# Kernel tuning notes

Measured on AMD Instinct MI355X. Metric: run time of the kernel, lower is better.

Reference implementation:

```python
import jax, jax.numpy as jnp
import numpy as np

EMBED_DIM = 768
MAX_LEN = 1024
ALPHA = 0.99
BATCH = 16


def setup_inputs() -> dict:
    key = jax.random.key(0)
    k1, k2, k3 = jax.random.split(key, 3)
    x = jax.random.normal(k1, (BATCH, MAX_LEN, EMBED_DIM), dtype=jnp.float32)
    # torch nn.Linear(embed_dim, 3*embed_dim): store weight as [in, out] for x @ W
    scale = 1.0 / np.sqrt(EMBED_DIM)
    W_qkv = jax.random.uniform(k2, (EMBED_DIM, 3 * EMBED_DIM), dtype=jnp.float32,
                               minval=-scale, maxval=scale)
    b_qkv = jax.random.uniform(k3, (3 * EMBED_DIM,), dtype=jnp.float32,
                               minval=-scale, maxval=scale)
    return {"x": x, "W_qkv": W_qkv, "b_qkv": b_qkv}


def _retention_mask(sl, alpha, dtype):
    # M[i, j] = alpha**(i - j) if i >= j else 0 (causal tril * decay)
    i = jnp.arange(sl)[:, None]
    j = jnp.arange(sl)[None, :]
    causal = i >= j
    # compute decay only where causal to avoid huge alpha**(negative) values
    exponent = jnp.where(causal, (i - j).astype(dtype), 0.0)
    decay = jnp.asarray(alpha, dtype) ** exponent
    return jnp.where(causal, decay, jnp.zeros((), dtype))


def reference(x, W_qkv, b_qkv):
    bs, sl, d = x.shape
    qkv = x @ W_qkv + b_qkv                      # [B, S, 3D]
    q, k, v = jnp.split(qkv, 3, axis=-1)         # each [B, S, D]
    M = _retention_mask(sl, ALPHA, x.dtype)      # [S, S]
    scores = jnp.einsum('bsd,btd->bst', q, k) / jnp.sqrt(jnp.asarray(d, x.dtype))
    out = jnp.einsum('bst,btd->bsd', scores * M[None, :, :], v)
    return out
```

## Files before the change

### kernel.cpp

```cpp
#include <hip/hip_runtime.h>
#include <hip/hip_bf16.h>


#define SEQ   1024
#define DIM   768
#define ND3   2304

typedef __attribute__((ext_vector_type(8))) short bf16x8;
typedef __attribute__((ext_vector_type(4))) float f32x4;

#define L2A     (-0.014499569695115089f)
#define RSQRTD  (0.03608439182435161f)

__device__ __forceinline__ unsigned short f2bf(float x) {
  union { float f; unsigned u; } v; v.f = x;
  unsigned r = v.u + 0x7FFFu + ((v.u >> 16) & 1u);
  return (unsigned short)(r >> 16);
}

__device__ __forceinline__ void gload16(const void* g, void* l) {
  __builtin_amdgcn_global_load_lds(
      (const __attribute__((address_space(1))) void*)g,
      (__attribute__((address_space(3))) void*)l, 16, 0, 0);
}

__global__ void prep(const float* __restrict__ x, unsigned short* __restrict__ xb,
                     const float* __restrict__ W, unsigned short* __restrict__ Wt) {
  __shared__ float tile[64][65];
  int bid = blockIdx.x;
  if (bid < 6144) {
    size_t i = ((size_t)bid * 256 + threadIdx.x) * 8;
    float4 f0 = *(const float4*)(x + i);
    float4 f1 = *(const float4*)(x + i + 4);
    bf16x8 v;
    v[0] = (short)f2bf(f0.x); v[1] = (short)f2bf(f0.y);
    v[2] = (short)f2bf(f0.z); v[3] = (short)f2bf(f0.w);
    v[4] = (short)f2bf(f1.x); v[5] = (short)f2bf(f1.y);
    v[6] = (short)f2bf(f1.z); v[7] = (short)f2bf(f1.w);
    *(bf16x8*)(xb + i) = v;
  } else {
    int tb = bid - 6144;
    int n0 = (tb % 36) * 64;
    int k0 = (tb / 36) * 64;
    int tx = threadIdx.x & 63, ty = threadIdx.x >> 6;
#pragma unroll
    for (int p = 0; p < 16; ++p) {
      int k = ty + p * 4;
      tile[k][tx] = W[(size_t)(k0 + k) * ND3 + n0 + tx];
    }
    __syncthreads();
#pragma unroll
    for (int p = 0; p < 16; ++p) {
      int n = ty + p * 4;
      Wt[(size_t)(n0 + n) * DIM + k0 + tx] = f2bf(tile[tx][n]);
    }
  }
}

__global__ void __launch_bounds__(512, 4) qkv_g(
    const unsigned short* __restrict__ xb, const unsigned short* __restrict__ Wt,
    const float* __restrict__ bias,
    unsigned short* __restrict__ Qs, unsigned short* __restrict__ Ks,
    unsigned short* __restrict__ Vt) {
  __shared__ __align__(1024) char lsA[16384];
  __shared__ __align__(1024) char lsB[32768];
  int bid = (blockIdx.x & 7) * 144 + (blockIdx.x >> 3);
  int mt = bid / 9, ntb = bid % 9;
  int m0 = mt * 128, n0 = ntb * 256;

  int tid = threadIdx.x, lane = tid & 63, wid = tid >> 6;
  int lr = lane & 15, lg = lane >> 4;
  int wm = wid >> 2, wn = wid & 3;
  int c8 = (lane & 7) ^ (lane >> 3);
  int rloc = (lane >> 3) * 2 + (c8 >> 2), colo = (c8 & 3) * 8;
  const unsigned short* gA = xb + (size_t)(m0 + rloc) * DIM + colo;
  const unsigned short* gB = Wt + (size_t)(n0 + rloc) * DIM + colo;
  int slot16 = (((((lr & 1) << 2) | lg) ^ ((lr >> 1) & 7)) << 4);
  int rdA = wm * 4096 + (lr >> 1) * 128 + slot16;
  int rdB = wn * 4096 + (lr >> 1) * 128 + slot16;

  f32x4 acc[4][4] = {};

#define STG(t, par) do {                                                      \
    char* la_ = lsA + (par) * 8192;                                           \
    char* lb_ = lsB + (par) * 16384;                                          \
    gload16(gA + (size_t)(wid * 16) * DIM + (t) * 32, la_ + wid * 1024);      \
    gload16(gB + (size_t)(wid * 32) * DIM + (t) * 32, lb_ + wid * 2048);      \
    gload16(gB + (size_t)(wid * 32 + 16) * DIM + (t) * 32,                    \
            lb_ + wid * 2048 + 1024);                                         \
  } while (0)

  STG(0, 0);
  STG(1, 1);
  asm volatile("s_waitcnt vmcnt(3)" ::: "memory");
  __builtin_amdgcn_s_barrier();
  asm volatile("" ::: "memory");

  for (int t = 0; t < 24; ++t) {
    int pA = (t & 1) * 8192, pB = (t & 1) * 16384;
    bf16x8 aF[4], bF[4];
#pragma unroll
    for (int f = 0; f < 4; ++f)
      aF[f] = *(const bf16x8*)(lsA + pA + rdA + f * 1024);
#pragma unroll
    for (int n = 0; n < 4; ++n)
      bF[n] = *(const bf16x8*)(lsB + pB + rdB + n * 1024);
    __builtin_amdgcn_s_setprio(1);
#pragma unroll
    for (int f = 0; f < 4; ++f)
#pragma unroll
      for (int n = 0; n < 4; ++n)
        acc[f][n] = __builtin_amdgcn_mfma_f32_16x16x32_bf16(aF[f], bF[n], acc[f][n], 0, 0, 0);
    __builtin_amdgcn_s_setprio(0);

    if (t == 23) break;
    __builtin_amdgcn_s_barrier();
    asm volatile("" ::: "memory");
    if (t + 2 < 24) {
      STG(t + 2, t & 1);
      asm volatile("s_waitcnt vmcnt(3)" ::: "memory");
    } else {
      asm volatile("s_waitcnt vmcnt(0)" ::: "memory");
    }
    __builtin_amdgcn_s_barrier();
    asm volatile("" ::: "memory");
  }
#undef STG

  float bia[4];
#pragma unroll
  for (int n = 0; n < 4; ++n) bia[n] = bias[n0 + wn * 64 + n * 16 + lr];

  if (ntb < 3) {
#pragma unroll
    for (int f = 0; f < 4; ++f)
#pragma unroll
      for (int r = 0; r < 4; ++r) {
        int mg = m0 + wm * 64 + f * 16 + lg * 4 + r;
        int b = mg >> 10, s = mg & 1023;
        float sc = exp2f((float)s * L2A) * RSQRTD;
        unsigned short* dst = Qs + ((size_t)b * SEQ + s) * DIM + n0 + wn * 64 + lr;
#pragma unroll
        for (int n = 0; n < 4; ++n)
          dst[n * 16] = f2bf((acc[f][n][r] + bia[n]) * sc);
      }
  } else if (ntb < 6) {
#pragma unroll
    for (int f = 0; f < 4; ++f)
#pragma unroll
      for (int r = 0; r < 4; ++r) {
        int mg = m0 + wm * 64 + f * 16 + lg * 4 + r;
        int b = mg >> 10, s = mg & 1023;
        float sc = exp2f(-(float)s * L2A);
        unsigned short* dst = Ks + ((size_t)b * SEQ + s) * DIM + (n0 - DIM) + wn * 64 + lr;
#pragma unroll
        for (int n = 0; n < 4; ++n)
          dst[n * 16] = f2bf((acc[f][n][r] + bia[n]) * sc);
      }
  } else {
#pragma unroll
    for (int f = 0; f < 4; ++f) {
      int mg = m0 + wm * 64 + f * 16 + lg * 4;
      int b = mg >> 10, s0 = mg & 1023;
#pragma unroll
      for (int n = 0; n < 4; ++n) {
        int d = (n0 - 2 * DIM) + wn * 64 + n * 16 + lr;
        ushort4 v;
        v.x = f2bf(acc[f][n][0] + bia[n]);
        v.y = f2bf(acc[f][n][1] + bia[n]);
        v.z = f2bf(acc[f][n][2] + bia[n]);
        v.w = f2bf(acc[f][n][3] + bia[n]);
        *(ushort4*)(Vt + ((size_t)b * DIM + d) * SEQ + s0) = v;
      }
    }
  }
}

__device__ __forceinline__ void gemm_core(
    const unsigned short* gA, const unsigned short* gA2,
    const unsigned short* gB, const unsigned short* gB2,
    char* lsA, char* lsB, int nt, int wid, int lane, f32x4 acc[2][4]) {
  int lr = lane & 15, lg = lane >> 4;
  int wm = wid >> 1, wn = wid & 1;
  int rdA = (wm * 32 + lr) * 128 + ((lg ^ (lr & 7)) << 4);
  int rdB = (wn * 64 + lr) * 128 + ((lg ^ (lr & 7)) << 4);
  int wo = wid * 2048;

#define STAGE(t, par) do {                                                    \
    int lo_ = ((par) << 14) + wo;                                             \
    gload16(gA  + (size_t)(t) * 64, lsA + lo_);                               \
    gload16(gA2 + (size_t)(t) * 64, lsA + lo_ + 1024);                        \
    gload16(gB  + (size_t)(t) * 64, lsB + lo_);                               \
    gload16(gB2 + (size_t)(t) * 64, lsB + lo_ + 1024);                        \
  } while (0)

  STAGE(0, 0);
  STAGE(1, 1);
  asm volatile("s_waitcnt vmcnt(4)" ::: "memory");
  __builtin_amdgcn_s_barrier();
  asm volatile("" ::: "memory");

  for (int t = 0; t < nt; ++t) {
    int pbase = (t & 1) << 14;
    bf16x8 aF[2][2], bF[2][4];
#pragma unroll
    for (int kh = 0; kh < 2; ++kh) {
#pragma unroll
      for (int f = 0; f < 2; ++f)
        aF[kh][f] = *(const bf16x8*)(lsA + pbase + ((rdA + f * 2048) ^ (kh << 6)));
#pragma unroll
      for (int n = 0; n < 4; ++n)
        bF[kh][n] = *(const bf16x8*)(lsB + pbase + ((rdB + n * 2048) ^ (kh << 6)));
    }
    __builtin_amdgcn_s_setprio(1);
#pragma unroll
    for (int kh = 0; kh < 2; ++kh)
#pragma unroll
      for (int f = 0; f < 2; ++f)
#pragma unroll
        for (int n = 0; n < 4; ++n)
          acc[f][n] = __builtin_amdgcn_mfma_f32_16x16x32_bf16(aF[kh][f], bF[kh][n], acc[f][n], 0, 0, 0);
    __builtin_amdgcn_s_setprio(0);

    if (t == nt - 1) break;
    __builtin_amdgcn_s_barrier();
    asm volatile("" ::: "memory");
    if (t + 2 < nt) {
      STAGE(t + 2, t & 1);
      asm volatile("s_waitcnt vmcnt(4)" ::: "memory");
    } else {
      asm volatile("s_waitcnt vmcnt(0)" ::: "memory");
    }
    __builtin_amdgcn_s_barrier();
    asm volatile("" ::: "memory");
  }
#undef STAGE
}

__global__ void __launch_bounds__(512, 4) score_g(
    const unsigned short* __restrict__ Qs, const unsigned short* __restrict__ Ks,
    unsigned short* __restrict__ Sm, int b_base) {
  __shared__ __align__(1024) char lsA[32768];
  __shared__ __align__(1024) char lsB[32768];
  int bid = (blockIdx.x & 7) * (gridDim.x >> 3) + (blockIdx.x >> 3);
  int t = bid % 36, bl = bid / 36;
  int b = b_base + bl;
  int it = 0;
  while (t >= it + 1) { t -= it + 1; it++; }
  int jt = t;
  int m0 = it * 128, n0 = jt * 128;
  const unsigned short* A  = Qs + (size_t)b * SEQ * DIM;
  const unsigned short* Bt = Ks + (size_t)b * SEQ * DIM;
  unsigned short* Smp = Sm + (size_t)bl * SEQ * SEQ;

  int tid = threadIdx.x, lane = tid & 63, wid = tid >> 6;
  int l8 = lane >> 3, cs = ((lane & 7) ^ l8) << 3;
  int srow = wid * 16 + l8;

  const unsigned short* gA = A  + (size_t)(m0 + srow) * DIM + cs;
  const unsigned short* gB = Bt + (size_t)(n0 + srow) * DIM + cs;

  f32x4 acc[2][4] = {};
  gemm_core(gA, gA + 8 * DIM, gB, gB + 8 * DIM, lsA, lsB, 12, wid, lane, acc);

  int wm = wid >> 1, wn = wid & 1;
  int lr = lane & 15, lg = lane >> 4;
#pragma unroll
  for (int f = 0; f < 2; ++f)
#pragma unroll
    for (int n = 0; n < 4; ++n) {
      int j = n0 + wn * 64 + n * 16 + lr;
#pragma unroll
      for (int r = 0; r < 4; ++r) {
        int i = m0 + wm * 32 + f * 16 + lg * 4 + r;
        float v = acc[f][n][r];
        if (j > i) v = 0.0f;
        Smp[(size_t)i * SEQ + j] = f2bf(v);
      }
    }
}

__global__ void __launch_bounds__(512, 4) pv_g(
    const unsigned short* __restrict__ Sm, const unsigned short* __restrict__ Vt,
    float* __restrict__ out, int b_base, int gsz) {
  __shared__ __align__(1024) char lsA[32768];
  __shared__ __align__(1024) char lsB[32768];
  int it = 7 - blockIdx.x / (gsz * 6);
  int rem = blockIdx.x % (gsz * 6);
  int bl = rem / 6, dt = rem % 6;
  int b = b_base + bl;
  int m0 = it * 128, n0 = dt * 128;
  const unsigned short* A  = Sm + (size_t)bl * SEQ * SEQ;
  const unsigned short* Bt = Vt + (size_t)b * DIM * SEQ;
  int nt = (it + 1) * 2;

  int tid = threadIdx.x, lane = tid & 63, wid = tid >> 6;
  int l8 = lane >> 3, cs = ((lane & 7) ^ l8) << 3;
  int srow = wid * 16 + l8;

  const unsigned short* gA = A  + (size_t)(m0 + srow) * SEQ + cs;
  const unsigned short* gB = Bt + (size_t)(n0 + srow) * SEQ + cs;

  f32x4 acc[2][4] = {};
  gemm_core(gA, gA + 8 * SEQ, gB, gB + 8 * SEQ, lsA, lsB, nt, wid, lane, acc);

  int wm = wid >> 1, wn = wid & 1;
  int lr = lane & 15, lg = lane >> 4;
#pragma unroll
  for (int f = 0; f < 2; ++f)
#pragma unroll
    for (int n = 0; n < 4; ++n) {
      int d = n0 + wn * 64 + n * 16 + lr;
#pragma unroll
      for (int r = 0; r < 4; ++r) {
        int i = m0 + wm * 32 + f * 16 + lg * 4 + r;
        out[((size_t)b * SEQ + i) * DIM + d] = acc[f][n][r];
      }
    }
}

extern "C" void kernel_launch(void* const* d_in, const int* in_sizes, int n_in,
                              void* d_out, int out_size, void* d_ws, size_t ws_size,
                              hipStream_t stream) {
  const float* x    = (const float*)d_in[0];
  const float* W    = (const float*)d_in[1];
  const float* bias = (const float*)d_in[2];
  float* out = (float*)d_out;

  char* ws = (char*)d_ws;
  unsigned short* Wt = (unsigned short*)(ws);
  unsigned short* Qs = (unsigned short*)(ws + 3538944);
  unsigned short* Ks = (unsigned short*)(ws + 3538944 + 25165824);
  unsigned short* Vt = (unsigned short*)(ws + 3538944 + 2 * 25165824);
  unsigned short* Sm = (unsigned short*)(ws + 3538944 + 3 * 25165824);
  unsigned short* xb = (unsigned short*)d_out;

  size_t smBase = 3538944 + 3 * (size_t)25165824;
  int gsz = (ws_size >= smBase + (size_t)16 * SEQ * SEQ * 2) ? 16 : 8;
  int ngrp = 16 / gsz;

  prep<<<6576, 256, 0, stream>>>(x, xb, W, Wt);
  qkv_g<<<1152, 512, 0, stream>>>(xb, Wt, bias, Qs, Ks, Vt);
  for (int g = 0; g < ngrp; ++g) {
    score_g<<<gsz * 36, 512, 0, stream>>>(Qs, Ks, Sm, g * gsz);
    pv_g<<<gsz * 48, 512, 0, stream>>>(Sm, Vt, out, g * gsz, gsz);
  }
}
```

Baseline: 152.3 us.

## Retile QKV GEMM to 128x192 tiles with K=64 stages and role-split loaders

Reshapes the QKV projection GEMM from 128x256 tiles with 8 waves to 128x192 tiles with 6 waves, and doubles the K step per pipeline stage to 64, halving the number of barrier-synchronised iterations. Loading is split by wave role: two waves stage the A tile and four stage the B tile, each with its own vmcnt gate. A new XOR swizzle is used for LDS reads. The 192-wide tiles line up with the Q/K/V boundaries at multiples of 768. In exchange, LDS per block grows to 80 KB, which limits occupancy, and load work is uneven across waves.

```diff
diff --git a/kernel.cpp b/kernel.cpp
--- a/kernel.cpp
+++ b/kernel.cpp
@@ -57,68 +57,85 @@
   }
 }
 
-__global__ void __launch_bounds__(512, 4) qkv_g(
+__global__ void __launch_bounds__(384, 3) qkv_g(
     const unsigned short* __restrict__ xb, const unsigned short* __restrict__ Wt,
     const float* __restrict__ bias,
     unsigned short* __restrict__ Qs, unsigned short* __restrict__ Ks,
     unsigned short* __restrict__ Vt) {
-  __shared__ __align__(1024) char lsA[16384];
-  __shared__ __align__(1024) char lsB[32768];
-  int bid = (blockIdx.x & 7) * 144 + (blockIdx.x >> 3);
-  int mt = bid / 9, ntb = bid % 9;
-  int m0 = mt * 128, n0 = ntb * 256;
+  __shared__ __align__(1024) char lsA[32768];
+  __shared__ __align__(1024) char lsB[49152];
+  int bid = (blockIdx.x & 7) * 192 + (blockIdx.x >> 3);
+  int mt = bid / 12, ntb = bid % 12;
+  int m0 = mt * 128, n0 = ntb * 192;
 
   int tid = threadIdx.x, lane = tid & 63, wid = tid >> 6;
   int lr = lane & 15, lg = lane >> 4;
-  int wm = wid >> 2, wn = wid & 3;
-  int c8 = (lane & 7) ^ (lane >> 3);
-  int rloc = (lane >> 3) * 2 + (c8 >> 2), colo = (c8 & 3) * 8;
-  const unsigned short* gA = xb + (size_t)(m0 + rloc) * DIM + colo;
-  const unsigned short* gB = Wt + (size_t)(n0 + rloc) * DIM + colo;
-  int slot16 = (((((lr & 1) << 2) | lg) ^ ((lr >> 1) & 7)) << 4);
-  int rdA = wm * 4096 + (lr >> 1) * 128 + slot16;
-  int rdB = wn * 4096 + (lr >> 1) * 128 + slot16;
+  int wm = wid / 3, wn = wid % 3;
+  int l8 = lane >> 3, cs = ((lane & 7) ^ l8) << 3;
+  const unsigned short* gS;
+  char* lbase;
+  int nld;
+  if (wid < 2) {
+    gS = xb + (size_t)(m0 + wid * 64 + l8) * DIM + cs;
+    lbase = lsA + wid * 8192;
+    nld = 8;
+  } else {
+    gS = Wt + (size_t)(n0 + (wid - 2) * 48 + l8) * DIM + cs;
+    lbase = lsB + (wid - 2) * 6144;
+    nld = 6;
+  }
+  int rdA = (wm * 64 + lr) * 128 + ((lg ^ (lr & 7)) << 4);
+  int rdB = (wn * 64 + lr) * 128 + ((lg ^ (lr & 7)) << 4);
 
   f32x4 acc[4][4] = {};
 
 #define STG(t, par) do {                                                      \
-    char* la_ = lsA + (par) * 8192;                                           \
-    char* lb_ = lsB + (par) * 16384;                                          \
-    gload16(gA + (size_t)(wid * 16) * DIM + (t) * 32, la_ + wid * 1024);      \
-    gload16(gB + (size_t)(wid * 32) * DIM + (t) * 32, lb_ + wid * 2048);      \
-    gload16(gB + (size_t)(wid * 32 + 16) * DIM + (t) * 32,                    \
-            lb_ + wid * 2048 + 1024);                                         \
+    char* d_ = lbase + (par) * ((wid < 2) ? 16384 : 24576);                   \
+    const unsigned short* s_ = gS + (size_t)(t) * 64;                         \
+    _Pragma("unroll")                                                         \
+    for (int i_ = 0; i_ < 8; ++i_)                                            \
+      if (i_ < nld)                                                           \
+        gload16(s_ + (size_t)(i_ * 8) * DIM, d_ + i_ * 1024);                 \
+  } while (0)
+#define GATE_ROLE do {                                                        \
+    if (wid < 2) { asm volatile("s_waitcnt vmcnt(8)" ::: "memory"); }         \
+    else         { asm volatile("s_waitcnt vmcnt(6)" ::: "memory"); }         \
   } while (0)
 
   STG(0, 0);
   STG(1, 1);
-  asm volatile("s_waitcnt vmcnt(3)" ::: "memory");
+  GATE_ROLE;
   __builtin_amdgcn_s_barrier();
   asm volatile("" ::: "memory");
 
-  for (int t = 0; t < 24; ++t) {
-    int pA = (t & 1) * 8192, pB = (t & 1) * 16384;
-    bf16x8 aF[4], bF[4];
-#pragma unroll
-    for (int f = 0; f < 4; ++f)
-      aF[f] = *(const bf16x8*)(lsA + pA + rdA + f * 1024);
-#pragma unroll
-    for (int n = 0; n < 4; ++n)
-      bF[n] = *(const bf16x8*)(lsB + pB + rdB + n * 1024);
+  for (int t = 0; t < 12; ++t) {
+    int pA = (t & 1) * 16384, pB = (t & 1) * 24576;
+    bf16x8 aF[2][4], bF[2][4];
+#pragma unroll
+    for (int kh = 0; kh < 2; ++kh) {
+#pragma unroll
+      for (int f = 0; f < 4; ++f)
+        aF[kh][f] = *(const bf16x8*)(lsA + pA + ((rdA + f * 2048) ^ (kh << 6)));
+#pragma unroll
+      for (int n = 0; n < 4; ++n)
+        bF[kh][n] = *(const bf16x8*)(lsB + pB + ((rdB + n * 2048) ^ (kh << 6)));
+    }
     __builtin_amdgcn_s_setprio(1);
 #pragma unroll
-    for (int f = 0; f < 4; ++f)
-#pragma unroll
-      for (int n = 0; n < 4; ++n)
-        acc[f][n] = __builtin_amdgcn_mfma_f32_16x16x32_bf16(aF[f], bF[n], acc[f][n], 0, 0, 0);
+    for (int kh = 0; kh < 2; ++kh)
+#pragma unroll
+      for (int f = 0; f < 4; ++f)
+#pragma unroll
+        for (int n = 0; n < 4; ++n)
+          acc[f][n] = __builtin_amdgcn_mfma_f32_16x16x32_bf16(aF[kh][f], bF[kh][n], acc[f][n], 0, 0, 0);
     __builtin_amdgcn_s_setprio(0);
 
-    if (t == 23) break;
+    if (t == 11) break;
     __builtin_amdgcn_s_barrier();
     asm volatile("" ::: "memory");
-    if (t + 2 < 24) {
+    if (t + 2 < 12) {
       STG(t + 2, t & 1);
-      asm volatile("s_waitcnt vmcnt(3)" ::: "memory");
+      GATE_ROLE;
     } else {
       asm volatile("s_waitcnt vmcnt(0)" ::: "memory");
     }
@@ -126,12 +143,13 @@
     asm volatile("" ::: "memory");
   }
 #undef STG
+#undef GATE_ROLE
 
   float bia[4];
 #pragma unroll
   for (int n = 0; n < 4; ++n) bia[n] = bias[n0 + wn * 64 + n * 16 + lr];
 
-  if (ntb < 3) {
+  if (ntb < 4) {
 #pragma unroll
     for (int f = 0; f < 4; ++f)
 #pragma unroll
@@ -144,7 +162,7 @@
         for (int n = 0; n < 4; ++n)
           dst[n * 16] = f2bf((acc[f][n][r] + bia[n]) * sc);
       }
-  } else if (ntb < 6) {
+  } else if (ntb < 8) {
 #pragma unroll
     for (int f = 0; f < 4; ++f)
 #pragma unroll
@@ -340,7 +358,7 @@
   int ngrp = 16 / gsz;
 
   prep<<<6576, 256, 0, stream>>>(x, xb, W, Wt);
-  qkv_g<<<1152, 512, 0, stream>>>(xb, Wt, bias, Qs, Ks, Vt);
+  qkv_g<<<1536, 384, 0, stream>>>(xb, Wt, bias, Qs, Ks, Vt);
   for (int g = 0; g < ngrp; ++g) {
     score_g<<<gsz * 36, 512, 0, stream>>>(Qs, Ks, Sm, g * gsz);
     pv_g<<<gsz * 48, 512, 0, stream>>>(Sm, Vt, out, g * gsz, gsz);
```

Result: slower. 158.5 us (+4.1%).
